# Performance work log

Hardware: AMD Instinct MI355X
Metric: run time of the kernel (lower is better)

Reference implementation:

```python
import math
import jax, jax.numpy as jnp
import numpy as np

B, S, DIM, H = 16, 1024, 1024, 16
HD = DIM // H            # head_dim = 64
ROPE_DIM = HD // 2       # 32; per-axis rotary dim
FT = 32                  # ft_seq_len, FT*FT == S
PT = 16                  # pt_seq_len
THETA = 10000.0
EPS = 1e-6


def _rope_cos_sin():
    # freqs_for='lang'
    freqs = 1.0 / THETA ** (jnp.arange(0, ROPE_DIM, 2, dtype=jnp.float32) / ROPE_DIM)  # [ROPE_DIM//2]
    t = jnp.arange(FT, dtype=jnp.float32) / FT * PT                                    # [FT]
    fs = jnp.einsum('n,f->nf', t, freqs)                                               # [FT, ROPE_DIM//2]
    fs = jnp.repeat(fs, 2, axis=-1)                                                    # [FT, ROPE_DIM]
    fh = jnp.broadcast_to(fs[:, None, :], (FT, FT, ROPE_DIM))
    fw = jnp.broadcast_to(fs[None, :, :], (FT, FT, ROPE_DIM))
    f = jnp.concatenate([fh, fw], axis=-1).reshape(-1, 2 * ROPE_DIM)                   # [S, HD]
    return jnp.cos(f), jnp.sin(f)


def _rotate_half(x):
    x1, x2 = jnp.split(x, 2, axis=-1)
    return jnp.concatenate((-x2, x1), axis=-1)


def _rms_norm(x, w):
    xf = x.astype(jnp.float32)
    var = jnp.mean(jnp.square(xf), axis=-1, keepdims=True)
    return (w * (xf * jax.lax.rsqrt(var + EPS))).astype(x.dtype)


def setup_inputs() -> dict:
    key = jax.random.key(0)
    ks = jax.random.split(key, 4)
    sd = 1.0 / math.sqrt(DIM)
    return {
        'x': jax.random.normal(ks[0], (B, S, DIM), dtype=jnp.float32),
        'w_qkv': jax.random.normal(ks[1], (DIM, 3 * DIM), dtype=jnp.float32) * sd,
        'b_qkv': jnp.zeros((3 * DIM,), dtype=jnp.float32),
        'q_norm_w': jnp.ones((HD,), dtype=jnp.float32),
        'k_norm_w': jnp.ones((HD,), dtype=jnp.float32),
        'w_out': jax.random.normal(ks[2], (DIM, DIM), dtype=jnp.float32) * sd,
        'b_out': jnp.zeros((DIM,), dtype=jnp.float32),
    }


def reference(x, w_qkv, b_qkv, q_norm_w, k_norm_w, w_out, b_out):
    cos, sin = _rope_cos_sin()                    # [S, HD] each
    cos = cos[None, None].astype(x.dtype)
    sin = sin[None, None].astype(x.dtype)

    qkv = x @ w_qkv + b_qkv                       # [B,S,3*DIM]
    qkv = qkv.reshape(B, S, 3, H, HD).transpose(2, 0, 3, 1, 4)  # [3,B,H,S,HD]
    q, k, v = qkv[0], qkv[1], qkv[2]

    q = _rms_norm(q, q_norm_w)
    k = _rms_norm(k, k_norm_w)

    q = q * cos + _rotate_half(q) * sin
    k = k * cos + _rotate_half(k) * sin

    scale = 1.0 / math.sqrt(HD)
    logits = jnp.einsum('bhqd,bhkd->bhqk', q.astype(jnp.float32), k.astype(jnp.float32)) * scale
    attn = jax.nn.softmax(logits, axis=-1).astype(x.dtype)
    out = jnp.einsum('bhqk,bhkd->bhqd', attn, v)  # [B,H,S,HD]

    out = out.transpose(0, 2, 1, 3).reshape(B, S, DIM)
    return out @ w_out + b_out
```

## Files before the change

kernel.cpp:

```cpp
#include <hip/hip_runtime.h>
#include <cstdint>
#include <cstddef>

#define B_    16
#define S_    1024
#define DIM_  1024
#define H_    16
#define HD_   64
#define TDIM  3072

typedef unsigned short ushort_t;
typedef unsigned int   uint_t;
typedef __attribute__((ext_vector_type(8)))  short s8v;
typedef __attribute__((ext_vector_type(4)))  float f32x4;
typedef __attribute__((ext_vector_type(16))) float f32x16;

__device__ __forceinline__ float b2f(ushort_t u) {
    union { uint_t i; float f; } t; t.i = (uint_t)u << 16; return t.f;
}
__device__ __forceinline__ ushort_t f2b(float f) {
    union { float f; uint_t i; } t; t.f = f;
    uint_t r = t.i + 0x7FFFu + ((t.i >> 16) & 1u);
    return (ushort_t)(r >> 16);
}
__device__ __forceinline__ uint_t cvt_pk_bf16(float a, float b) {
    uint_t r;
    asm("v_cvt_pk_bf16_f32 %0, %1, %2" : "=v"(r) : "v"(a), "v"(b));
    return r;
}

__device__ __forceinline__ f32x4 mfma_bf16(s8v a, s8v b, f32x4 c) {
    asm volatile("v_mfma_f32_16x16x32_bf16 %0, %1, %2, %0" : "+v"(c) : "v"(a), "v"(b));
    return c;
}
__device__ __forceinline__ f32x16 mfma32_bf16(s8v a, s8v b, f32x16 c) {
    asm volatile("v_mfma_f32_32x32x16_bf16 %0, %1, %2, %0" : "+v"(c) : "v"(a), "v"(b));
    return c;
}

__device__ __forceinline__ void gload16(const void* g, void* l) {
    __builtin_amdgcn_global_load_lds(
        (const __attribute__((address_space(1))) uint_t*)g,
        (__attribute__((address_space(3))) uint_t*)l, 16, 0, 0);
}

__device__ __forceinline__ void bar() {
    asm volatile("" ::: "memory");
    __builtin_amdgcn_s_barrier();
    asm volatile("" ::: "memory");
}
__device__ __forceinline__ void wait_vm0() {
    asm volatile("s_waitcnt vmcnt(0)" ::: "memory");
}
__device__ __forceinline__ void wait_vm4() {
    asm volatile("s_waitcnt vmcnt(4)" ::: "memory");
}

__device__ __forceinline__ void transpose_job(const float* __restrict__ Wsrc,
                                              short* __restrict__ WT,
                                              int K, int N, int bx, int by,
                                              float (*t)[33]) {
    int tx = threadIdx.x & 31, ty = threadIdx.x >> 5;
    int n0 = bx * 32, k0 = by * 32;
#pragma unroll
    for (int i = 0; i < 4; ++i)
        t[ty + 8 * i][tx] = Wsrc[(size_t)(k0 + ty + 8 * i) * N + n0 + tx];
    __syncthreads();
#pragma unroll
    for (int i = 0; i < 4; ++i)
        WT[(size_t)(n0 + ty + 8 * i) * K + k0 + tx] = (short)f2b(t[tx][ty + 8 * i]);
}

__global__ __launch_bounds__(256) void prep_all(const float* __restrict__ x,
                                                short* __restrict__ xb,
                                                const float* __restrict__ w_qkv,
                                                short* __restrict__ wqkvT,
                                                const float* __restrict__ w_out,
                                                short* __restrict__ woutT,
                                                float* __restrict__ cos_t,
                                                float* __restrict__ sin_t) {
    __shared__ float t[32][33];
    const int bid = blockIdx.x;
    if (bid < 8192) {
        int i = bid * 256 + threadIdx.x;
        float4 a = *(const float4*)(x + (size_t)i * 8);
        float4 b = *(const float4*)(x + (size_t)i * 8 + 4);
        s8v v;
        v[0] = (short)f2b(a.x); v[1] = (short)f2b(a.y);
        v[2] = (short)f2b(a.z); v[3] = (short)f2b(a.w);
        v[4] = (short)f2b(b.x); v[5] = (short)f2b(b.y);
        v[6] = (short)f2b(b.z); v[7] = (short)f2b(b.w);
        *(s8v*)(xb + (size_t)i * 8) = v;
    } else if (bid < 11264) {
        int idx = bid - 8192;
        transpose_job(w_qkv, wqkvT, 1024, 3072, idx % 96, idx / 96, t);
    } else if (bid < 12288) {
        int idx = bid - 11264;
        transpose_job(w_out, woutT, 1024, 1024, idx % 32, idx / 32, t);
    } else {
        int idx = (bid - 12288) * 256 + threadIdx.x;
        int s = idx >> 6;
        int d = idx & 63;
        int pos = (d < 32) ? (s >> 5) : (s & 31);
        int i   = (d & 31) >> 1;
        float freq  = expf(-(float)i * 0.5756462732485115f);
        float angle = (float)pos * 0.5f * freq;
        cos_t[idx] = cosf(angle);
        sin_t[idx] = sinf(angle);
    }
}

template<typename CT, bool NORM>
__global__ __launch_bounds__(512) void gemm8ph(
        const short* __restrict__ A, const short* __restrict__ BT,
        const float* __restrict__ bias, CT* __restrict__ C,
        int M, int N, int K, int NX,
        const float* __restrict__ qw, const float* __restrict__ kw,
        const float* __restrict__ cos_t, const float* __restrict__ sin_t) {
    __shared__ short As[2][256 * 64];
    __shared__ short Bs[3][256 * 64];

    const int tid  = threadIdx.x;
    const int w    = tid >> 6;
    const int lane = tid & 63;
    const int l15  = lane & 15, lg = lane >> 4;
    const int wm = w >> 2, wn = w & 3;

    const int nwg  = gridDim.x;
    const int cpx  = nwg >> 3;
    const int wgid = (blockIdx.x & 7) * cpx + (blockIdx.x >> 3);
    const int bx = wgid % NX, by = wgid / NX;
    const int m0 = by * 256, n0 = bx * 256;

    const int NT = K >> 6;

    const int sgrow = w * 8 + (lane >> 3);
    const int ksrc  = (((lane & 7) ^ (lane >> 3)) * 8);

    auto stageA = [&](int t, int buf) {
        const size_t k0 = (size_t)t * 64;
#pragma unroll
        for (int j = 0; j < 4; ++j)
            gload16(A + (size_t)(m0 + j * 64 + sgrow) * K + k0 + ksrc,
                    &As[buf][(j * 64 + w * 8) * 64]);
    };
    auto stageB = [&](int t, int buf) {
        const size_t k0 = (size_t)t * 64;
#pragma unroll
        for (int j = 0; j < 4; ++j)
            gload16(BT + (size_t)(n0 + j * 64 + sgrow) * K + k0 + ksrc,
                    &Bs[buf][(j * 64 + w * 8) * 64]);
    };

    const int swz = l15 & 7;

    auto rdA = [&](int buf, int mh, s8v (&dst)[4][2]) {
#pragma unroll
        for (int i = 0; i < 4; ++i) {
            int row = wm * 128 + mh * 64 + i * 16 + l15;
#pragma unroll
            for (int kk = 0; kk < 2; ++kk)
                dst[i][kk] = *(const s8v*)&As[buf][row * 64 + (((kk * 4 + lg) ^ swz) * 8)];
        }
    };
    auto rdB = [&](int buf, int nh, s8v (&dst)[4][2]) {
#pragma unroll
        for (int ni = 0; ni < 2; ++ni) {
            int row = wn * 64 + (nh * 2 + ni) * 16 + l15;
#pragma unroll
            for (int kk = 0; kk < 2; ++kk)
                dst[nh * 2 + ni][kk] = *(const s8v*)&Bs[buf][row * 64 + (((kk * 4 + lg) ^ swz) * 8)];
        }
    };

    stageA(0, 0);
    stageB(0, 0);
    stageB(1, 1);
    wait_vm4();
    bar();

    s8v a0[4][2], a1[4][2], bb[4][2];
    rdA(0, 0, a0);
    rdB(0, 0, bb);
    rdB(0, 1, bb);
    rdA(0, 1, a1);

    f32x4 acc[8][4] = {};

    int bufB = 0;
    for (int t = 0; t < NT; ++t) {
        const int bufA  = t & 1;
        const int nbufB = (bufB == 2) ? 0 : bufB + 1;
        const int sbufB = (nbufB == 2) ? 0 : nbufB + 1;

        if (t + 1 < NT) stageA(t + 1, bufA ^ 1);
        if (t + 2 < NT) stageB(t + 2, sbufB);

        __builtin_amdgcn_s_setprio(1);
#pragma unroll
        for (int i = 0; i < 4; ++i)
#pragma unroll
            for (int ni = 0; ni < 2; ++ni)
#pragma unroll
                for (int kk = 0; kk < 2; ++kk)
                    acc[i][ni] = mfma_bf16(a0[i][kk], bb[ni][kk], acc[i][ni]);
        __builtin_amdgcn_s_setprio(0);

        __builtin_amdgcn_s_setprio(1);
#pragma unroll
        for (int i = 0; i < 4; ++i)
#pragma unroll
            for (int ni = 2; ni < 4; ++ni)
#pragma unroll
                for (int kk = 0; kk < 2; ++kk)
                    acc[i][ni] = mfma_bf16(a0[i][kk], bb[ni][kk], acc[i][ni]);
        __builtin_amdgcn_s_setprio(0);

        __builtin_amdgcn_s_setprio(1);
#pragma unroll
        for (int i = 0; i < 4; ++i)
#pragma unroll
            for (int ni = 0; ni < 2; ++ni)
#pragma unroll
                for (int kk = 0; kk < 2; ++kk)
                    acc[4 + i][ni] = mfma_bf16(a1[i][kk], bb[ni][kk], acc[4 + i][ni]);
        __builtin_amdgcn_s_setprio(0);

        if (t < NT - 2) wait_vm4(); else wait_vm0();
        bar();

        if (t + 1 < NT) {
            rdA(bufA ^ 1, 0, a0);
            rdB(nbufB, 0, bb);
        }

        __builtin_amdgcn_s_setprio(1);
#pragma unroll
        for (int i = 0; i < 4; ++i)
#pragma unroll
            for (int ni = 2; ni < 4; ++ni)
#pragma unroll
                for (int kk = 0; kk < 2; ++kk)
                    acc[4 + i][ni] = mfma_bf16(a1[i][kk], bb[ni][kk], acc[4 + i][ni]);
        __builtin_amdgcn_s_setprio(0);

        if (t + 1 < NT) {
            rdB(nbufB, 1, bb);
            rdA(bufA ^ 1, 1, a1);
        }
        bufB = nbufB;
    }

    const int colbase = n0 + wn * 64;
    if constexpr (NORM) {
        if (colbase < 2048) {
            const float* nw = (colbase < 1024) ? qw : kw;
            float wv[4], bv[4];
#pragma unroll
            for (int ni = 0; ni < 4; ++ni) {
                wv[ni] = nw[16 * ni + l15];
                bv[ni] = bias[colbase + 16 * ni + l15];
            }
#pragma unroll
            for (int mi = 0; mi < 8; ++mi) {
#pragma unroll
                for (int r = 0; r < 4; ++r) {
                    int row = m0 + wm * 128 + mi * 16 + lg * 4 + r;
                    int s = row & (S_ - 1);
                    float v[4];
#pragma unroll
                    for (int ni = 0; ni < 4; ++ni) v[ni] = acc[mi][ni][r] + bv[ni];
                    float ss = v[0]*v[0] + v[1]*v[1] + v[2]*v[2] + v[3]*v[3];
                    ss += __shfl_xor(ss, 1);
                    ss += __shfl_xor(ss, 2);
                    ss += __shfl_xor(ss, 4);
                    ss += __shfl_xor(ss, 8);
                    float rms = rsqrtf(ss * (1.0f / 64.0f) + 1e-6f);
                    float xn[4];
#pragma unroll
                    for (int ni = 0; ni < 4; ++ni) xn[ni] = v[ni] * rms * wv[ni];
#pragma unroll
                    for (int ni = 0; ni < 4; ++ni) {
                        int d = 16 * ni + l15;
                        float c  = cos_t[s * 64 + d];
                        float sn = sin_t[s * 64 + d];
                        float rot = (ni < 2) ? -xn[ni + 2] : xn[ni - 2];
                        C[(size_t)row * N + colbase + d] = (short)f2b(xn[ni] * c + rot * sn);
                    }
                }
            }
            return;
        }
    }
#pragma unroll
    for (int ni = 0; ni < 4; ++ni) {
        float bvv = bias[colbase + 16 * ni + l15];
#pragma unroll
        for (int mi = 0; mi < 8; ++mi) {
#pragma unroll
            for (int r = 0; r < 4; ++r) {
                size_t row = (size_t)(m0 + wm * 128 + mi * 16 + lg * 4 + r);
                int    col = colbase + 16 * ni + l15;
                float v = acc[mi][ni][r] + bvv;
                if constexpr (sizeof(CT) == 4) C[row * N + col] = v;
                else                           C[row * N + col] = (short)f2b(v);
            }
        }
    }
}

__global__ __launch_bounds__(256) void attn_mfma(const short* __restrict__ qkv,
                                                 short* __restrict__ attn) {
    __shared__ ushort_t pool[8192];

    const float SC = 0.18033688011112042f;
    const float M_ = 12.0f;

    const int tid  = threadIdx.x;
    const int w    = tid >> 6;
    const int lane = tid & 63;
    const int l31  = lane & 31, l5 = lane >> 5;

    const int bid = blockIdx.x;
    const int xcd = bid & 7;
    const int jj_ = bid >> 3;
    const int bh  = xcd * 32 + (jj_ >> 3);
    const int b   = bh >> 4, h = bh & 15;
    const int q0  = (jj_ & 7) * 128;

    const short* qbase = qkv + (size_t)b * S_ * TDIM + h * HD_;
    const short* kb_ = qbase + DIM_;
    const short* vb_ = qbase + 2 * DIM_;

    ushort_t* Ks = pool;
    ushort_t* Vt = pool + 4096;

    s8v qf[4];
#pragma unroll
    for (int kc = 0; kc < 4; ++kc)
        qf[kc] = *(const s8v*)(qbase + (size_t)(q0 + w * 32 + l31) * TDIM + kc * 16 + l5 * 8);

    f32x16 of0 = {}, of1 = {};
    float l_s = 0.f;

    const int kr   = tid >> 3;
    const int kch  = (((tid & 7) ^ (kr & 7)) << 3);
    const int va   = tid & 7;
    const int vkp  = tid >> 3;
    const int vp8  = va * 8;
    const int k2    = 2 * vkp;
    const int kperm = (k2 & 0x33) | ((k2 & 4) << 1) | ((k2 & 8) >> 1);
    const int rsw   = l31 & 7;
    const int vrx   = (l31 & 7) ^ (l31 >> 3);

    s8v kA, kB, vA, vB;
    auto prefetch = [&](int kt) {
        const short* kbt = kb_ + (size_t)kt * 64 * TDIM;
        const short* vbt = vb_ + (size_t)kt * 64 * TDIM;
        kA = *(const s8v*)(kbt + (size_t)kr * TDIM + (tid & 7) * 8);
        kB = *(const s8v*)(kbt + (size_t)(kr + 32) * TDIM + (tid & 7) * 8);
        vA = *(const s8v*)(vbt + (size_t)k2 * TDIM + vp8);
        vB = *(const s8v*)(vbt + (size_t)(k2 + 1) * TDIM + vp8);
    };
    prefetch(0);

    for (int kt = 0; kt < 16; ++kt) {
        *(s8v*)&Ks[kr * 64 + kch]        = kA;
        *(s8v*)&Ks[(kr + 32) * 64 + kch] = kB;
#pragma unroll
        for (int j = 0; j < 8; ++j) {
            uint_t pk = (ushort_t)vA[j] | ((uint_t)(ushort_t)vB[j] << 16);
            int pcol = ((((kperm >> 3) ^ j ^ va) << 3) | (kperm & 7));
            *(uint_t*)&Vt[(vp8 + j) * 64 + pcol] = pk;
        }
        __syncthreads();

        if (kt < 15) prefetch(kt + 1);

        f32x16 st0 = {}, st1 = {};
        __builtin_amdgcn_s_setprio(1);
#pragma unroll
        for (int kc = 0; kc < 4; ++kc) {
            int pc = (((2 * kc + l5) ^ rsw) << 3);
            s8v kf0 = *(const s8v*)&Ks[l31 * 64 + pc];
            s8v kf1 = *(const s8v*)&Ks[(32 + l31) * 64 + pc];
            st0 = mfma32_bf16(kf0, qf[kc], st0);
            st1 = mfma32_bf16(kf1, qf[kc], st1);
        }
        __builtin_amdgcn_s_setprio(0);

        float la = 0.f, lb = 0.f, lc = 0.f, ld = 0.f;
#pragma unroll
        for (int r = 0; r < 16; r += 2) {
            float p00 = exp2f(__builtin_fmaf(st0[r],     SC, -M_));
            float p01 = exp2f(__builtin_fmaf(st0[r + 1], SC, -M_));
            float p10 = exp2f(__builtin_fmaf(st1[r],     SC, -M_));
            float p11 = exp2f(__builtin_fmaf(st1[r + 1], SC, -M_));
            st0[r] = p00; st0[r + 1] = p01;
            st1[r] = p10; st1[r + 1] = p11;
            la += p00; lb += p01; lc += p10; ld += p11;
        }
        float ls = (la + lb) + (lc + ld);
        ls += __shfl_xor(ls, 32);
        l_s += ls;

        uint_t P20[8], P21[8];
#pragma unroll
        for (int i = 0; i < 8; ++i) {
            P20[i] = cvt_pk_bf16(st0[2 * i], st0[2 * i + 1]);
            P21[i] = cvt_pk_bf16(st1[2 * i], st1[2 * i + 1]);
        }

        __builtin_amdgcn_s_setprio(1);
#pragma unroll
        for (int kb = 0; kb < 2; ++kb) {
            const uint_t* P2 = kb ? P21 : P20;
#pragma unroll
            for (int c = 0; c < 2; ++c) {
                union { uint_t u[4]; s8v v; } pf;
                pf.u[0] = P2[4 * c + 0];
                pf.u[1] = P2[4 * c + 1];
                pf.u[2] = P2[4 * c + 2];
                pf.u[3] = P2[4 * c + 3];

                int pc0 = (((4 * kb + 2 * c + l5) ^ vrx) << 3);
                int pc1 = pc0 ^ 32;
                s8v vf0 = *(const s8v*)&Vt[l31 * 64 + pc0];
                s8v vf1 = *(const s8v*)&Vt[(32 + l31) * 64 + pc1];
                of0 = mfma32_bf16(vf0, pf.v, of0);
                of1 = mfma32_bf16(vf1, pf.v, of1);
            }
        }
        __builtin_amdgcn_s_setprio(0);
        __syncthreads();
    }

    float inv = 1.0f / l_s;
    ushort_t* OL = pool + w * 2048;
#pragma unroll
    for (int r = 0; r < 16; r += 2) {
        int d = (r & 3) + 8 * (r >> 2) + 4 * l5;
        uint_t p0 = cvt_pk_bf16(of0[r] * inv, of0[r + 1] * inv);
        uint_t p1 = cvt_pk_bf16(of1[r] * inv, of1[r + 1] * inv);
        int c0 = d, c1 = 32 + d;
        int pc0 = (((c0 >> 3) ^ (l31 & 7)) << 3) | (c0 & 7);
        int pc1 = (((c1 >> 3) ^ (l31 & 7)) << 3) | (c1 & 7);
        *(uint_t*)&OL[l31 * 64 + pc0] = p0;
        *(uint_t*)&OL[l31 * 64 + pc1] = p1;
    }
#pragma unroll
    for (int i = 0; i < 4; ++i) {
        int idx = lane + i * 64;
        int row = idx >> 3, ch = idx & 7;
        int pch = ((ch ^ (row & 7)) << 3);
        *(s8v*)&attn[((size_t)b * S_ + q0 + w * 32 + row) * DIM_ + h * HD_ + ch * 8] =
            *(const s8v*)&OL[row * 64 + pch];
    }
}

extern "C" void kernel_launch(void* const* d_in, const int* in_sizes, int n_in,
                              void* d_out, int out_size, void* d_ws, size_t ws_size,
                              hipStream_t stream) {
    const float* x        = (const float*)d_in[0];
    const float* w_qkv    = (const float*)d_in[1];
    const float* b_qkv    = (const float*)d_in[2];
    const float* q_norm_w = (const float*)d_in[3];
    const float* k_norm_w = (const float*)d_in[4];
    const float* w_out    = (const float*)d_in[5];
    const float* b_out    = (const float*)d_in[6];
    float* out = (float*)d_out;

    const size_t OFF_QKV = 0;
    const size_t OFF_ATT = 100663296;
    const size_t OFF_XB  = OFF_ATT + 33554432;
    const size_t OFF_WQ  = OFF_XB + 33554432;
    const size_t OFF_WO  = OFF_WQ + 6291456;
    const size_t OFF_CT  = OFF_WO + 2097152;
    const size_t OFF_ST  = OFF_CT + 262144;
    const size_t NEED    = OFF_ST + 262144;

    if (ws_size < NEED) {
        hipMemsetAsync(d_out, 0, (size_t)out_size * sizeof(float), stream);
        return;
    }

    char* ws = (char*)d_ws;
    short* qkv   = (short*)(ws + OFF_QKV);
    short* attnb = (short*)(ws + OFF_ATT);
    short* xb    = (short*)(ws + OFF_XB);
    short* wqkvT = (short*)(ws + OFF_WQ);
    short* woutT = (short*)(ws + OFF_WO);
    float* cos_t = (float*)(ws + OFF_CT);
    float* sin_t = (float*)(ws + OFF_ST);

    prep_all<<<dim3(12544), dim3(256), 0, stream>>>(
        x, xb, w_qkv, wqkvT, w_out, woutT, cos_t, sin_t);

    gemm8ph<short, true><<<dim3(768), dim3(512), 0, stream>>>(
        xb, wqkvT, b_qkv, qkv, 16384, 3072, 1024, 12,
        q_norm_w, k_norm_w, cos_t, sin_t);

    attn_mfma<<<dim3(2048), dim3(256), 0, stream>>>(qkv, attnb);

    gemm8ph<float, false><<<dim3(256), dim3(512), 0, stream>>>(
        attnb, woutT, b_out, out, 16384, 1024, 1024, 4,
        nullptr, nullptr, nullptr, nullptr);
}
```

Before: 277.1 us.

## Replace 256x256 GEMM tile with 128x128 tile and simpler double buffering

```diff
diff --git a/kernel.cpp b/kernel.cpp
--- a/kernel.cpp
+++ b/kernel.cpp
@@ -111,26 +111,26 @@
 }
 
 template<typename CT, bool NORM>
-__global__ __launch_bounds__(512) void gemm8ph(
+__global__ __launch_bounds__(256) void gemm128(
         const short* __restrict__ A, const short* __restrict__ BT,
         const float* __restrict__ bias, CT* __restrict__ C,
         int M, int N, int K, int NX,
         const float* __restrict__ qw, const float* __restrict__ kw,
         const float* __restrict__ cos_t, const float* __restrict__ sin_t) {
-    __shared__ short As[2][256 * 64];
-    __shared__ short Bs[3][256 * 64];
+    __shared__ short As[2][128 * 64];
+    __shared__ short Bs[2][128 * 64];
 
     const int tid  = threadIdx.x;
     const int w    = tid >> 6;
     const int lane = tid & 63;
     const int l15  = lane & 15, lg = lane >> 4;
-    const int wm = w >> 2, wn = w & 3;
+    const int wm = w >> 1, wn = w & 1;
 
     const int nwg  = gridDim.x;
     const int cpx  = nwg >> 3;
     const int wgid = (blockIdx.x & 7) * cpx + (blockIdx.x >> 3);
     const int bx = wgid % NX, by = wgid / NX;
-    const int m0 = by * 256, n0 = bx * 256;
+    const int m0 = by * 128, n0 = bx * 128;
 
     const int NT = K >> 6;
 
@@ -141,114 +141,82 @@
         const size_t k0 = (size_t)t * 64;
 #pragma unroll
         for (int j = 0; j < 4; ++j)
-            gload16(A + (size_t)(m0 + j * 64 + sgrow) * K + k0 + ksrc,
-                    &As[buf][(j * 64 + w * 8) * 64]);
+            gload16(A + (size_t)(m0 + j * 32 + sgrow) * K + k0 + ksrc,
+                    &As[buf][(j * 32 + w * 8) * 64]);
     };
     auto stageB = [&](int t, int buf) {
         const size_t k0 = (size_t)t * 64;
 #pragma unroll
         for (int j = 0; j < 4; ++j)
-            gload16(BT + (size_t)(n0 + j * 64 + sgrow) * K + k0 + ksrc,
-                    &Bs[buf][(j * 64 + w * 8) * 64]);
+            gload16(BT + (size_t)(n0 + j * 32 + sgrow) * K + k0 + ksrc,
+                    &Bs[buf][(j * 32 + w * 8) * 64]);
     };
 
     const int swz = l15 & 7;
 
-    auto rdA = [&](int buf, int mh, s8v (&dst)[4][2]) {
-#pragma unroll
-        for (int i = 0; i < 4; ++i) {
-            int row = wm * 128 + mh * 64 + i * 16 + l15;
+    s8v af[4][2], bf[4][2];
+    auto rdA = [&](int buf, int half) {
+#pragma unroll
+        for (int i = 0; i < 2; ++i) {
+            int row = wm * 64 + (half * 2 + i) * 16 + l15;
 #pragma unroll
             for (int kk = 0; kk < 2; ++kk)
-                dst[i][kk] = *(const s8v*)&As[buf][row * 64 + (((kk * 4 + lg) ^ swz) * 8)];
+                af[half * 2 + i][kk] =
+                    *(const s8v*)&As[buf][row * 64 + (((kk * 4 + lg) ^ swz) * 8)];
         }
     };
-    auto rdB = [&](int buf, int nh, s8v (&dst)[4][2]) {
+    auto rdB = [&](int buf, int half) {
 #pragma unroll
         for (int ni = 0; ni < 2; ++ni) {
-            int row = wn * 64 + (nh * 2 + ni) * 16 + l15;
+            int row = wn * 64 + (half * 2 + ni) * 16 + l15;
 #pragma unroll
             for (int kk = 0; kk < 2; ++kk)
-                dst[nh * 2 + ni][kk] = *(const s8v*)&Bs[buf][row * 64 + (((kk * 4 + lg) ^ swz) * 8)];
+                bf[half * 2 + ni][kk] =
+                    *(const s8v*)&Bs[buf][row * 64 + (((kk * 4 + lg) ^ swz) * 8)];
         }
     };
 
     stageA(0, 0);
     stageB(0, 0);
-    stageB(1, 1);
-    wait_vm4();
+    wait_vm0();
     bar();
-
-    s8v a0[4][2], a1[4][2], bb[4][2];
-    rdA(0, 0, a0);
-    rdB(0, 0, bb);
-    rdB(0, 1, bb);
-    rdA(0, 1, a1);
-
-    f32x4 acc[8][4] = {};
-
-    int bufB = 0;
+    rdA(0, 0); rdA(0, 1);
+    rdB(0, 0); rdB(0, 1);
+
+    f32x4 acc[4][4] = {};
+
     for (int t = 0; t < NT; ++t) {
-        const int bufA  = t & 1;
-        const int nbufB = (bufB == 2) ? 0 : bufB + 1;
-        const int sbufB = (nbufB == 2) ? 0 : nbufB + 1;
-
-        if (t + 1 < NT) stageA(t + 1, bufA ^ 1);
-        if (t + 2 < NT) stageB(t + 2, sbufB);
+        const int buf = t & 1;
+        const bool more = (t + 1 < NT);
+
+        if (more) { stageA(t + 1, buf ^ 1); stageB(t + 1, buf ^ 1); }
 
         __builtin_amdgcn_s_setprio(1);
 #pragma unroll
-        for (int i = 0; i < 4; ++i)
-#pragma unroll
-            for (int ni = 0; ni < 2; ++ni)
+        for (int i = 0; i < 2; ++i)
+#pragma unroll
+            for (int ni = 0; ni < 4; ++ni)
 #pragma unroll
                 for (int kk = 0; kk < 2; ++kk)
-                    acc[i][ni] = mfma_bf16(a0[i][kk], bb[ni][kk], acc[i][ni]);
+                    acc[i][ni] = mfma_bf16(af[i][kk], bf[ni][kk], acc[i][ni]);
         __builtin_amdgcn_s_setprio(0);
 
+        wait_vm0();
+        bar();
+
+        if (more) rdA(buf ^ 1, 0);
+
         __builtin_amdgcn_s_setprio(1);
 #pragma unroll
-        for (int i = 0; i < 4; ++i)
-#pragma unroll
-            for (int ni = 2; ni < 4; ++ni)
+        for (int i = 2; i < 4; ++i)
+#pragma unroll
+            for (int ni = 0; ni < 4; ++ni)
 #pragma unroll
                 for (int kk = 0; kk < 2; ++kk)
-                    acc[i][ni] = mfma_bf16(a0[i][kk], bb[ni][kk], acc[i][ni]);
+                    acc[i][ni] = mfma_bf16(af[i][kk], bf[ni][kk], acc[i][ni]);
         __builtin_amdgcn_s_setprio(0);
 
-        __builtin_amdgcn_s_setprio(1);
-#pragma unroll
-        for (int i = 0; i < 4; ++i)
-#pragma unroll
-            for (int ni = 0; ni < 2; ++ni)
-#pragma unroll
-                for (int kk = 0; kk < 2; ++kk)
-                    acc[4 + i][ni] = mfma_bf16(a1[i][kk], bb[ni][kk], acc[4 + i][ni]);
-        __builtin_amdgcn_s_setprio(0);
-
-        if (t < NT - 2) wait_vm4(); else wait_vm0();
-        bar();
-
-        if (t + 1 < NT) {
-            rdA(bufA ^ 1, 0, a0);
-            rdB(nbufB, 0, bb);
-        }
-
-        __builtin_amdgcn_s_setprio(1);
-#pragma unroll
-        for (int i = 0; i < 4; ++i)
-#pragma unroll
-            for (int ni = 2; ni < 4; ++ni)
-#pragma unroll
-                for (int kk = 0; kk < 2; ++kk)
-                    acc[4 + i][ni] = mfma_bf16(a1[i][kk], bb[ni][kk], acc[4 + i][ni]);
-        __builtin_amdgcn_s_setprio(0);
-
-        if (t + 1 < NT) {
-            rdB(nbufB, 1, bb);
-            rdA(bufA ^ 1, 1, a1);
-        }
-        bufB = nbufB;
+        if (more) { rdA(buf ^ 1, 1); rdB(buf ^ 1, 0); rdB(buf ^ 1, 1); }
     }
 
     const int colbase = n0 + wn * 64;
@@ -262,10 +230,10 @@
                 bv[ni] = bias[colbase + 16 * ni + l15];
             }
 #pragma unroll
-            for (int mi = 0; mi < 8; ++mi) {
+            for (int mi = 0; mi < 4; ++mi) {
 #pragma unroll
                 for (int r = 0; r < 4; ++r) {
-                    int row = m0 + wm * 128 + mi * 16 + lg * 4 + r;
+                    int row = m0 + wm * 64 + mi * 16 + lg * 4 + r;
                     int s = row & (S_ - 1);
                     float v[4];
 #pragma unroll
@@ -296,10 +264,10 @@
     for (int ni = 0; ni < 4; ++ni) {
         float bvv = bias[colbase + 16 * ni + l15];
 #pragma unroll
-        for (int mi = 0; mi < 8; ++mi) {
+        for (int mi = 0; mi < 4; ++mi) {
 #pragma unroll
             for (int r = 0; r < 4; ++r) {
-                size_t row = (size_t)(m0 + wm * 128 + mi * 16 + lg * 4 + r);
+                size_t row = (size_t)(m0 + wm * 64 + mi * 16 + lg * 4 + r);
                 int    col = colbase + 16 * ni + l15;
                 float v = acc[mi][ni][r] + bvv;
                 if constexpr (sizeof(CT) == 4) C[row * N + col] = v;
@@ -496,13 +464,13 @@
     prep_all<<<dim3(12544), dim3(256), 0, stream>>>(
         x, xb, w_qkv, wqkvT, w_out, woutT, cos_t, sin_t);
 
-    gemm8ph<short, true><<<dim3(768), dim3(512), 0, stream>>>(
-        xb, wqkvT, b_qkv, qkv, 16384, 3072, 1024, 12,
+    gemm128<short, true><<<dim3(3072), dim3(256), 0, stream>>>(
+        xb, wqkvT, b_qkv, qkv, 16384, 3072, 1024, 24,
         q_norm_w, k_norm_w, cos_t, sin_t);
 
     attn_mfma<<<dim3(2048), dim3(256), 0, stream>>>(qkv, attnb);
 
-    gemm8ph<float, false><<<dim3(256), dim3(512), 0, stream>>>(
-        attnb, woutT, b_out, out, 16384, 1024, 1024, 4,
+    gemm128<float, false><<<dim3(1024), dim3(256), 0, stream>>>(
+        attnb, woutT, b_out, out, 16384, 1024, 1024, 8,
         nullptr, nullptr, nullptr, nullptr);
 }
```

Result: slower. 302.8 us (+9.3%).
